# Performance work log

Measured on AMD Instinct MI355X. Metric: run time of the kernel, lower is better.

The kernel has to match this reference:

```python
import jax, jax.numpy as jnp
import numpy as np

HEADS = 4
DIM_HEAD = 128
DIM = 128
INNER = HEADS * DIM_HEAD  # 512
MAX_POS = 100
SCALE = DIM_HEAD ** -0.5


def setup_inputs() -> dict:
    key = jax.random.key(0)
    ks = jax.random.split(key, 8)
    b, h, w = 2, 48, 64
    fmap1 = jax.random.normal(ks[0], (b, DIM, h, w), jnp.float32)
    fmap2 = jax.random.normal(ks[1], (b, DIM, h, w), jnp.float32)
    Wqk = jax.random.normal(ks[2], (2 * INNER, DIM), jnp.float32) * 0.05
    Wv = jax.random.normal(ks[3], (INNER, DIM), jnp.float32) * 0.05
    rel_h = jax.random.normal(ks[4], (2 * MAX_POS - 1, DIM_HEAD), jnp.float32) * 0.05
    rel_w = jax.random.normal(ks[5], (2 * MAX_POS - 1, DIM_HEAD), jnp.float32) * 0.05
    Wp = jax.random.normal(ks[6], (DIM, INNER), jnp.float32) * 0.05
    gamma = jnp.full((1,), 0.1, jnp.float32)  # nonzero so the attn path is active
    return {"fmap1": fmap1, "fmap2": fmap2, "Wqk": Wqk, "Wv": Wv,
            "rel_h": rel_h, "rel_w": rel_w, "Wp": Wp, "gamma": gamma}


def _aggregate(fmap, Wqk, Wv, rel_h, rel_w, Wp, gamma):
    b, c, H, W = fmap.shape
    # 1x1 conv = channel matmul
    qk = jnp.einsum('oc,bchw->bohw', Wqk, fmap)
    q = qk[:, :INNER] * SCALE  # k chunk unused (position-only similarity)
    # b (n d) h w -> b n h w d
    q = q.reshape(b, HEADS, DIM_HEAD, H, W).transpose(0, 1, 3, 4, 2)
    v = jnp.einsum('oc,bchw->bohw', Wv, fmap)
    v = v.reshape(b, HEADS, DIM_HEAD, H, W).transpose(0, 1, 3, 4, 2).reshape(b, HEADS, H * W, DIM_HEAD)
    # relative position similarity (RelPosEmb)
    idx_h = jnp.arange(H)[:, None] - jnp.arange(H)[None, :] + (MAX_POS - 1)  # (H,H)
    idx_w = jnp.arange(W)[:, None] - jnp.arange(W)[None, :] + (MAX_POS - 1)  # (W,W)
    He = rel_h[idx_h]  # (x,u,d)
    We = rel_w[idx_w]  # (y,v,d)
    hs = jnp.einsum('bnxyd,xud->bnxyu', q, He)  # (b,n,x,y,u)
    ws = jnp.einsum('bnxyd,yvd->bnxyv', q, We)  # (b,n,x,y,v)
    sim = hs[..., :, None] + ws[..., None, :]   # (b,n,x,y,u,v)
    sim = sim.reshape(b, HEADS, H * W, H * W)
    attn = jax.nn.softmax(sim, axis=-1)
    out = jnp.einsum('bnij,bnjd->bnid', attn, v)  # (b,n,hw,d)
    out = out.reshape(b, HEADS, H, W, DIM_HEAD).transpose(0, 1, 4, 2, 3).reshape(b, INNER, H, W)
    out = jnp.einsum('oc,bchw->bohw', Wp, out)  # project (dim != inner_dim)
    return fmap + gamma[0] * out


def reference(fmap1, fmap2, Wqk, Wv, rel_h, rel_w, Wp, gamma):
    out1 = _aggregate(fmap1, Wqk, Wv, rel_h, rel_w, Wp, gamma)
    out2 = _aggregate(fmap2, Wqk, Wv, rel_h, rel_w, Wp, gamma)
    return (out1, out2)
```

## Files before the change

kernel.cpp:

```cpp
#include <hip/hip_runtime.h>
#include <cstdint>
#include <cstddef>

typedef short bf16x8 __attribute__((ext_vector_type(8)));
typedef float f32x4 __attribute__((ext_vector_type(4)));

#define HH 48
#define WW 64
#define HWSZ 3072
#define SCALE_Q 0.08838834764831845f

__device__ __forceinline__ float b2f(unsigned short u) {
    union { unsigned int i; float f; } c; c.i = ((unsigned int)u) << 16; return c.f;
}
__device__ __forceinline__ unsigned short f2b(float f) {
    union { float f; unsigned int i; } c; c.f = f;
    unsigned int r = (c.i + 0x7fffu + ((c.i >> 16) & 1u)) >> 16;
    return (unsigned short)r;
}

__device__ __forceinline__ void dma16(const unsigned short* g, unsigned short* l) {
    __builtin_amdgcn_global_load_lds((const __attribute__((address_space(1))) unsigned int*)g,
                                     (__attribute__((address_space(3))) unsigned int*)l,
                                     16, 0, 0);
}

__global__ __launch_bounds__(256) void k_transpose(const float* __restrict__ f0,
                                                   const float* __restrict__ f1,
                                                   unsigned short* __restrict__ Xb) {
    __shared__ float t[32][33];
    int fb = blockIdx.z; int f = fb >> 1, bb = fb & 1;
    const float* src = f ? f1 : f0;
    int pT = blockIdx.x * 32, cT = blockIdx.y * 32;
    int tx = threadIdx.x, ty = threadIdx.y;
#pragma unroll
    for (int i = 0; i < 4; ++i) {
        int c = cT + ty + i * 8, pos = pT + tx;
        t[ty + i * 8][tx] = src[(size_t)(bb * 128 + c) * HWSZ + pos];
    }
    __syncthreads();
#pragma unroll
    for (int i = 0; i < 4; ++i) {
        int pos = pT + ty + i * 8, c = cT + tx;
        Xb[(size_t)(fb * HWSZ + pos) * 128 + c] = f2b(t[tx][ty + i * 8]);
    }
}

__global__ __launch_bounds__(256) void k_weights(const float* __restrict__ Wqk,
                                                 const float* __restrict__ Wv,
                                                 const float* __restrict__ Wp,
                                                 unsigned short* __restrict__ Wcat,
                                                 unsigned short* __restrict__ Wpb) {
    int idx = blockIdx.x * 256 + threadIdx.x;
    if (idx < 131072) {
        int o = idx >> 7, c = idx & 127;
        float v = (o < 512) ? Wqk[o * 128 + c] * SCALE_Q : Wv[(o - 512) * 128 + c];
        Wcat[idx] = f2b(v);
    } else {
        int j = idx - 131072;
        Wpb[j] = f2b(Wp[j]);
    }
}

__global__ __launch_bounds__(256) void k_qv(const unsigned short* __restrict__ Xb,
                                            const unsigned short* __restrict__ Wcat,
                                            unsigned short* __restrict__ Qx,
                                            unsigned short* __restrict__ Vt) {
    __shared__ unsigned short Asub[64 * 136];
    __shared__ unsigned short Bsub[128 * 136];
    int mt = blockIdx.x, nt = blockIdx.y, fb = blockIdx.z;
    int tid = threadIdx.x;
    const unsigned short* asrc = Xb + (size_t)(fb * HWSZ + mt * 64) * 128;
    const unsigned short* bsrc = Wcat + (size_t)nt * 128 * 128;
    for (int ch = tid; ch < 1024; ch += 256) {
        int row = ch >> 4, seg = ch & 15;
        *(bf16x8*)&Asub[row * 136 + seg * 8] = *(const bf16x8*)(asrc + ch * 8);
    }
    for (int ch = tid; ch < 2048; ch += 256) {
        int row = ch >> 4, seg = ch & 15;
        *(bf16x8*)&Bsub[row * 136 + seg * 8] = *(const bf16x8*)(bsrc + ch * 8);
    }
    __syncthreads();
    int l = tid & 63, w = tid >> 6;
    int wm = w >> 1, wn = w & 1;
    int lr = l & 15, lk8 = (l >> 4) * 8;
    f32x4 acc[2][4] = {};
#pragma unroll
    for (int kt = 0; kt < 4; ++kt) {
        bf16x8 a[2], b[4];
#pragma unroll
        for (int m = 0; m < 2; ++m)
            a[m] = *(const bf16x8*)&Asub[(wm * 32 + m * 16 + lr) * 136 + kt * 32 + lk8];
#pragma unroll
        for (int n = 0; n < 4; ++n)
            b[n] = *(const bf16x8*)&Bsub[(wn * 64 + n * 16 + lr) * 136 + kt * 32 + lk8];
#pragma unroll
        for (int m = 0; m < 2; ++m)
#pragma unroll
            for (int n = 0; n < 4; ++n)
                acc[m][n] = __builtin_amdgcn_mfma_f32_16x16x32_bf16(a[m], b[n], acc[m][n], 0, 0, 0);
    }
    int f = fb >> 1, bb = fb & 1;
#pragma unroll
    for (int m = 0; m < 2; ++m)
#pragma unroll
        for (int n = 0; n < 4; ++n) {
            int o = nt * 128 + wn * 64 + n * 16 + lr;
            int pos0 = mt * 64 + wm * 32 + m * 16 + (l >> 4) * 4;
            if (o < 512) {
                int nh = o >> 7, d = o & 127;
#pragma unroll
                for (int r = 0; r < 4; ++r) {
                    int pos = pos0 + r, x = pos >> 6, y = pos & 63;
                    Qx[(size_t)((f * 48 + x) * 512 + (bb * 4 + nh) * 64 + y) * 128 + d] = f2b(acc[m][n][r]);
                }
            } else {
                int oo = o - 512, nh = oo >> 7, d = oo & 127;
                int u = pos0 >> 6, v = pos0 & 63;
                uint2 val;
                val.x = (unsigned int)f2b(acc[m][n][0]) | ((unsigned int)f2b(acc[m][n][1]) << 16);
                val.y = (unsigned int)f2b(acc[m][n][2]) | ((unsigned int)f2b(acc[m][n][3]) << 16);
                *(uint2*)&Vt[(((size_t)(fb * 4 + nh) * 48 + u) * 128 + d) * 64 + v] = val;
            }
        }
}

__global__ __launch_bounds__(256) void k_ph(const unsigned short* __restrict__ Qx,
                                            const float* __restrict__ rel_h,
                                            unsigned short* __restrict__ PH) {
    __shared__ float sm[4][16][52];
    int x = blockIdx.x, f = blockIdx.y, mtz = blockIdx.z;
    int tid = threadIdx.x, l = tid & 63, w = tid >> 6;
    int lr = l & 15, lk8 = (l >> 4) * 8;
    bf16x8 bh[3][4];
#pragma unroll
    for (int ut = 0; ut < 3; ++ut) {
        int u = ut * 16 + lr, rr = x - u + 99;
#pragma unroll
        for (int kt = 0; kt < 4; ++kt) {
            const float* s = rel_h + rr * 128 + kt * 32 + lk8;
            float4 a0 = *(const float4*)s, a1 = *(const float4*)(s + 4);
            bf16x8 pk;
            pk[0] = (short)f2b(a0.x); pk[1] = (short)f2b(a0.y); pk[2] = (short)f2b(a0.z); pk[3] = (short)f2b(a0.w);
            pk[4] = (short)f2b(a1.x); pk[5] = (short)f2b(a1.y); pk[6] = (short)f2b(a1.z); pk[7] = (short)f2b(a1.w);
            bh[ut][kt] = pk;
        }
    }
    const unsigned short* qbase = Qx + (size_t)(f * 48 + x) * 512 * 128;
    unsigned short* phbase = PH + (size_t)(f * 48 + x) * 512 * 48;
    for (int mt = mtz * 2; mt < mtz * 2 + 2; ++mt) {
        int rg = w * 128 + mt * 16 + lr;
        const unsigned short* qrow = qbase + (size_t)rg * 128;
        bf16x8 a[4];
#pragma unroll
        for (int kt = 0; kt < 4; ++kt) a[kt] = *(const bf16x8*)(qrow + kt * 32 + lk8);
        f32x4 acc[3] = {};
#pragma unroll
        for (int kt = 0; kt < 4; ++kt)
#pragma unroll
            for (int ut = 0; ut < 3; ++ut)
                acc[ut] = __builtin_amdgcn_mfma_f32_16x16x32_bf16(a[kt], bh[ut][kt], acc[ut], 0, 0, 0);
        __syncthreads();
#pragma unroll
        for (int ut = 0; ut < 3; ++ut)
#pragma unroll
            for (int r = 0; r < 4; ++r)
                sm[w][(l >> 4) * 4 + r][ut * 16 + lr] = acc[ut][r];
        __syncthreads();
        int part = l >> 4;
        float vb[12];
        float mx = -1e30f;
#pragma unroll
        for (int j = 0; j < 12; ++j) { vb[j] = sm[w][lr][part * 12 + j]; mx = fmaxf(mx, vb[j]); }
        mx = fmaxf(mx, __shfl_xor(mx, 16, 64));
        mx = fmaxf(mx, __shfl_xor(mx, 32, 64));
        float ssum = 0.f;
#pragma unroll
        for (int j = 0; j < 12; ++j) { vb[j] = __expf(vb[j] - mx); ssum += vb[j]; }
        ssum += __shfl_xor(ssum, 16, 64);
        ssum += __shfl_xor(ssum, 32, 64);
        float inv = 1.0f / ssum;
        unsigned short* dst = phbase + (size_t)(w * 128 + mt * 16 + lr) * 48 + part * 12;
#pragma unroll
        for (int j = 0; j < 12; ++j) dst[j] = f2b(vb[j] * inv);
    }
}

__global__ __launch_bounds__(256) void k_pw(const unsigned short* __restrict__ Qx,
                                            const float* __restrict__ rel_w,
                                            unsigned short* __restrict__ PW) {
    __shared__ float sm[4][16][68];
    int y = blockIdx.x, f = blockIdx.y, mtz = blockIdx.z;
    int tid = threadIdx.x, l = tid & 63, w = tid >> 6;
    int lr = l & 15, lk8 = (l >> 4) * 8;
    bf16x8 bw[4][4];
#pragma unroll
    for (int vt = 0; vt < 4; ++vt) {
        int v = vt * 16 + lr, rr = y - v + 99;
#pragma unroll
        for (int kt = 0; kt < 4; ++kt) {
            const float* s = rel_w + rr * 128 + kt * 32 + lk8;
            float4 a0 = *(const float4*)s, a1 = *(const float4*)(s + 4);
            bf16x8 pk;
            pk[0] = (short)f2b(a0.x); pk[1] = (short)f2b(a0.y); pk[2] = (short)f2b(a0.z); pk[3] = (short)f2b(a0.w);
            pk[4] = (short)f2b(a1.x); pk[5] = (short)f2b(a1.y); pk[6] = (short)f2b(a1.z); pk[7] = (short)f2b(a1.w);
            bw[vt][kt] = pk;
        }
    }
    for (int mt = mtz * 2; mt < mtz * 2 + 2; ++mt) {
        int rg = w * 96 + mt * 16 + lr;
        int bn = rg / 48, xx = rg - bn * 48;
        const unsigned short* qrow = Qx + (size_t)((f * 48 + xx) * 512 + bn * 64 + y) * 128;
        bf16x8 a[4];
#pragma unroll
        for (int kt = 0; kt < 4; ++kt) a[kt] = *(const bf16x8*)(qrow + kt * 32 + lk8);
        f32x4 acc[4] = {};
#pragma unroll
        for (int kt = 0; kt < 4; ++kt)
#pragma unroll
            for (int vt = 0; vt < 4; ++vt)
                acc[vt] = __builtin_amdgcn_mfma_f32_16x16x32_bf16(a[kt], bw[vt][kt], acc[vt], 0, 0, 0);
        __syncthreads();
#pragma unroll
        for (int vt = 0; vt < 4; ++vt)
#pragma unroll
            for (int r = 0; r < 4; ++r)
                sm[w][(l >> 4) * 4 + r][vt * 16 + lr] = acc[vt][r];
        __syncthreads();
        int part = l >> 4;
        float vb[16];
        float mx = -1e30f;
#pragma unroll
        for (int j = 0; j < 16; ++j) { vb[j] = sm[w][lr][part * 16 + j]; mx = fmaxf(mx, vb[j]); }
        mx = fmaxf(mx, __shfl_xor(mx, 16, 64));
        mx = fmaxf(mx, __shfl_xor(mx, 32, 64));
        float ssum = 0.f;
#pragma unroll
        for (int j = 0; j < 16; ++j) { vb[j] = __expf(vb[j] - mx); ssum += vb[j]; }
        ssum += __shfl_xor(ssum, 16, 64);
        ssum += __shfl_xor(ssum, 32, 64);
        float inv = 1.0f / ssum;
        unsigned short* dst = PW + (size_t)((f * 64 + y) * 384 + rg) * 64 + part * 16;
#pragma unroll
        for (int j = 0; j < 16; ++j) dst[j] = f2b(vb[j] * inv);
    }
}

__global__ __launch_bounds__(256, 3) void k_attn(const unsigned short* __restrict__ PH,
                                                 const unsigned short* __restrict__ PW,
                                                 const unsigned short* __restrict__ Vt,
                                                 unsigned short* __restrict__ AO) {
    __shared__ unsigned short phl[48 * 128];
    __shared__ unsigned short vbuf[2][4096];
    int bid = blockIdx.x;
    int r16 = bid & 15;
    int rest = bid >> 4;
    int t = rest >> 1, dh = rest & 1;
    int fbn = (r16 & 7) * 2 + (r16 >> 3);
    int f = fbn >> 3, bidx = (fbn >> 2) & 1, nh = fbn & 3;
    int fb = f * 2 + bidx, bn = bidx * 4 + nh;
    int tid = threadIdx.x;
    int l = tid & 63, wd = tid >> 6;
    int lr = l & 15, lg = l >> 4, lk8 = lg * 8;

    const unsigned short* vhalf = Vt + (size_t)(fb * 4 + nh) * 48 * 8192 + dh * 4096;
    int r0 = wd * 16 + (l >> 3), s0 = l & 7;
    int r1 = r0 + 8;
    int g0 = r0 * 64 + ((s0 ^ (r0 & 7)) * 8);
    int g1 = r1 * 64 + ((s0 ^ (r1 & 7)) * 8);

#define DMA_U(BUF, U)                                                           \
    {                                                                           \
        const unsigned short* gt = vhalf + (size_t)(U) * 8192;                  \
        dma16(gt + g0, &vbuf[BUF][wd * 1024]);                                  \
        dma16(gt + g1, &vbuf[BUF][wd * 1024 + 512]);                            \
    }

    DMA_U(0, 0);

    for (int i = tid; i < 3072; i += 256) {
        int up2 = i >> 7, q = i & 127;
        int xy = t * 128 + q, x = xy >> 6, y = xy & 63;
        unsigned int wv = *(const unsigned int*)(PH + ((size_t)(f * 48 + x) * 512 + bn * 64 + y) * 48 + up2 * 2);
        int qoff = (q & 15) * 8 + (q >> 4);
        phl[(up2 * 2) * 128 + qoff]     = (unsigned short)(wv & 0xffffu);
        phl[(up2 * 2 + 1) * 128 + qoff] = (unsigned short)(wv >> 16);
    }
    bf16x8 b[8][2];
#pragma unroll
    for (int n = 0; n < 8; ++n) {
        int xy = t * 128 + n * 16 + lr;
        int x = xy >> 6, y = xy & 63;
        const unsigned short* pwr = PW + ((size_t)(f * 64 + y) * 384 + bn * 48 + x) * 64;
        b[n][0] = *(const bf16x8*)(pwr + lk8);
        b[n][1] = *(const bf16x8*)(pwr + 32 + lk8);
    }
    asm volatile("s_waitcnt vmcnt(0)" ::: "memory");
    __syncthreads();

    int arow = wd * 16 + lr;
    int ao0 = arow * 64 + ((lg ^ (arow & 7)) * 8);
    int ao1 = arow * 64 + (((4 + lg) ^ (arow & 7)) * 8);
    const unsigned short* phrow = &phl[lr * 8];
    f32x4 acc[8] = {};
    const f32x4 zero4 = {0.f, 0.f, 0.f, 0.f};

    int buf = 0;
    for (int u = 0; u < 48; ++u) {
        if (u + 1 < 48) DMA_U(buf ^ 1, u + 1);
        bf16x8 av0 = *(const bf16x8*)&vbuf[buf][ao0];
        bf16x8 av1 = *(const bf16x8*)&vbuf[buf][ao1];
        bf16x8 phv = *(const bf16x8*)(phrow + u * 128);
        __builtin_amdgcn_s_setprio(1);
#pragma unroll
        for (int n = 0; n < 8; ++n) {
            f32x4 Y = __builtin_amdgcn_mfma_f32_16x16x32_bf16(av0, b[n][0], zero4, 0, 0, 0);
            Y = __builtin_amdgcn_mfma_f32_16x16x32_bf16(av1, b[n][1], Y, 0, 0, 0);
            acc[n] += b2f((unsigned short)phv[n]) * Y;
        }
        __builtin_amdgcn_s_setprio(0);
        asm volatile("s_waitcnt vmcnt(0)" ::: "memory");
        __syncthreads();
        buf ^= 1;
    }
#undef DMA_U

    unsigned short* aobase = AO + (size_t)fb * HWSZ * 512 + nh * 128 + dh * 64 + wd * 16 + lg * 4;
#pragma unroll
    for (int n = 0; n < 8; ++n) {
        int q = t * 128 + n * 16 + lr;
        uint2 val;
        val.x = (unsigned int)f2b(acc[n][0]) | ((unsigned int)f2b(acc[n][1]) << 16);
        val.y = (unsigned int)f2b(acc[n][2]) | ((unsigned int)f2b(acc[n][3]) << 16);
        *(uint2*)(aobase + (size_t)q * 512) = val;
    }
}

__global__ __launch_bounds__(256) void k_proj(const unsigned short* __restrict__ AO,
                                              const unsigned short* __restrict__ Wpb,
                                              const float* __restrict__ f0,
                                              const float* __restrict__ f1,
                                              const float* __restrict__ gamma,
                                              float* __restrict__ out) {
    __shared__ unsigned short Asub[32 * 136];
    __shared__ unsigned short Bsub[128 * 136];
    int t = blockIdx.x, fb = blockIdx.y;
    int f = fb >> 1, bb = fb & 1;
    int tid = threadIdx.x;
    int l = tid & 63, w = tid >> 6;
    int wm = w >> 1, wn = w & 1;
    int lr = l & 15, lk8 = (l >> 4) * 8;
    f32x4 acc[4] = {};
    for (int ks = 0; ks < 4; ++ks) {
        if (ks) __syncthreads();
        for (int ch = tid; ch < 512; ch += 256) {
            int row = ch >> 4, seg = ch & 15;
            *(bf16x8*)&Asub[row * 136 + seg * 8] =
                *(const bf16x8*)(AO + (size_t)(fb * HWSZ + t * 32 + row) * 512 + ks * 128 + seg * 8);
        }
        for (int ch = tid; ch < 2048; ch += 256) {
            int row = ch >> 4, seg = ch & 15;
            *(bf16x8*)&Bsub[row * 136 + seg * 8] =
                *(const bf16x8*)(Wpb + (size_t)row * 512 + ks * 128 + seg * 8);
        }
        __syncthreads();
#pragma unroll
        for (int kt = 0; kt < 4; ++kt) {
            bf16x8 a, b[4];
            a = *(const bf16x8*)&Asub[(wm * 16 + lr) * 136 + kt * 32 + lk8];
#pragma unroll
            for (int n = 0; n < 4; ++n)
                b[n] = *(const bf16x8*)&Bsub[(wn * 64 + n * 16 + lr) * 136 + kt * 32 + lk8];
#pragma unroll
            for (int n = 0; n < 4; ++n)
                acc[n] = __builtin_amdgcn_mfma_f32_16x16x32_bf16(a, b[n], acc[n], 0, 0, 0);
        }
    }
    const float* fmapf = f ? f1 : f0;
    float g = gamma[0];
#pragma unroll
    for (int n = 0; n < 4; ++n) {
        int c = wn * 64 + n * 16 + lr;
        int pos0 = t * 32 + wm * 16 + (l >> 4) * 4;
        size_t addr = (size_t)(bb * 128 + c) * HWSZ + pos0;
        float4 fv = *(const float4*)(fmapf + addr);
        float4 ov;
        ov.x = fv.x + g * acc[n][0];
        ov.y = fv.y + g * acc[n][1];
        ov.z = fv.z + g * acc[n][2];
        ov.w = fv.w + g * acc[n][3];
        *(float4*)(out + (size_t)f * 786432 + addr) = ov;
    }
}

extern "C" void kernel_launch(void* const* d_in, const int* in_sizes, int n_in,
                              void* d_out, int out_size, void* d_ws, size_t ws_size,
                              hipStream_t stream) {
    (void)in_sizes; (void)n_in; (void)out_size; (void)ws_size;
    const float* fmap1 = (const float*)d_in[0];
    const float* fmap2 = (const float*)d_in[1];
    const float* Wqk   = (const float*)d_in[2];
    const float* Wv    = (const float*)d_in[3];
    const float* rel_h = (const float*)d_in[4];
    const float* rel_w = (const float*)d_in[5];
    const float* Wp    = (const float*)d_in[6];
    const float* gamma = (const float*)d_in[7];
    float* out = (float*)d_out;
    char* ws = (char*)d_ws;

    unsigned short* Xb   = (unsigned short*)(ws + 0);
    unsigned short* Wcat = (unsigned short*)(ws + 3145728);
    unsigned short* Wpb  = (unsigned short*)(ws + 3407872);
    unsigned short* Qx   = (unsigned short*)(ws + 3538944);
    unsigned short* AO   = Qx;
    unsigned short* Vt   = (unsigned short*)(ws + 16121856);
    unsigned short* PH   = (unsigned short*)(ws + 28704768);
    unsigned short* PW   = (unsigned short*)(ws + 33423360);

    k_transpose<<<dim3(96, 4, 4), dim3(32, 8), 0, stream>>>(fmap1, fmap2, Xb);
    k_weights<<<dim3(768), dim3(256), 0, stream>>>(Wqk, Wv, Wp, Wcat, Wpb);
    k_qv<<<dim3(48, 8, 4), dim3(256), 0, stream>>>(Xb, Wcat, Qx, Vt);
    k_ph<<<dim3(48, 2, 4), dim3(256), 0, stream>>>(Qx, rel_h, PH);
    k_pw<<<dim3(64, 2, 3), dim3(256), 0, stream>>>(Qx, rel_w, PW);
    k_attn<<<dim3(768), dim3(256), 0, stream>>>(PH, PW, Vt, AO);
    k_proj<<<dim3(96, 4), dim3(256), 0, stream>>>(AO, Wpb, fmap1, fmap2, gamma, out);
}
```

Before: 116.7 us.

## Store V in plain channel-major layout and stage via registers instead of LDS DMA

The V projection now writes V as [fb,head,d,HW] instead of a per-row tiled layout. The attention kernel loads each next 64x64 V tile into registers with ordinary global loads and writes it, swizzled, into the alternate LDS buffer after the MFMA work, replacing global_load_lds DMA. The setprio hints are removed. This trades the async DMA path for register staging, which costs extra VGPRs and LDS write instructions and reads strided rows of HWSZ.

```diff
diff --git a/kernel.cpp b/kernel.cpp
--- a/kernel.cpp
+++ b/kernel.cpp
@@ -17,12 +17,6 @@
     union { float f; unsigned int i; } c; c.f = f;
     unsigned int r = (c.i + 0x7fffu + ((c.i >> 16) & 1u)) >> 16;
     return (unsigned short)r;
-}
-
-__device__ __forceinline__ void dma16(const unsigned short* g, unsigned short* l) {
-    __builtin_amdgcn_global_load_lds((const __attribute__((address_space(1))) unsigned int*)g,
-                                     (__attribute__((address_space(3))) unsigned int*)l,
-                                     16, 0, 0);
 }
 
 __global__ __launch_bounds__(256) void k_transpose(const float* __restrict__ f0,
@@ -116,11 +110,10 @@
                 }
             } else {
                 int oo = o - 512, nh = oo >> 7, d = oo & 127;
-                int u = pos0 >> 6, v = pos0 & 63;
                 uint2 val;
                 val.x = (unsigned int)f2b(acc[m][n][0]) | ((unsigned int)f2b(acc[m][n][1]) << 16);
                 val.y = (unsigned int)f2b(acc[m][n][2]) | ((unsigned int)f2b(acc[m][n][3]) << 16);
-                *(uint2*)&Vt[(((size_t)(fb * 4 + nh) * 48 + u) * 128 + d) * 64 + v] = val;
+                *(uint2*)&Vt[(size_t)((fb * 4 + nh) * 128 + d) * HWSZ + pos0] = val;
             }
         }
 }
@@ -251,7 +244,7 @@
                                                  const unsigned short* __restrict__ Vt,
                                                  unsigned short* __restrict__ AO) {
     __shared__ unsigned short phl[48 * 128];
-    __shared__ unsigned short vbuf[2][4096];
+    __shared__ unsigned short vbuf[2][64 * 64];
     int bid = blockIdx.x;
     int r16 = bid & 15;
     int rest = bid >> 4;
@@ -263,20 +256,15 @@
     int l = tid & 63, wd = tid >> 6;
     int lr = l & 15, lg = l >> 4, lk8 = lg * 8;
 
-    const unsigned short* vhalf = Vt + (size_t)(fb * 4 + nh) * 48 * 8192 + dh * 4096;
-    int r0 = wd * 16 + (l >> 3), s0 = l & 7;
-    int r1 = r0 + 8;
-    int g0 = r0 * 64 + ((s0 ^ (r0 & 7)) * 8);
-    int g1 = r1 * 64 + ((s0 ^ (r1 & 7)) * 8);
-
-#define DMA_U(BUF, U)                                                           \
-    {                                                                           \
-        const unsigned short* gt = vhalf + (size_t)(U) * 8192;                  \
-        dma16(gt + g0, &vbuf[BUF][wd * 1024]);                                  \
-        dma16(gt + g1, &vbuf[BUF][wd * 1024 + 512]);                            \
-    }
-
-    DMA_U(0, 0);
+    const unsigned short* vsrc = Vt + (size_t)((fb * 4 + nh) * 128 + dh * 64) * HWSZ;
+    int sd = tid >> 3, sch = tid & 7;
+    const unsigned short* vsrow0 = vsrc + (size_t)sd * HWSZ + sch * 8;
+    const unsigned short* vsrow1 = vsrc + (size_t)(sd + 32) * HWSZ + sch * 8;
+    int wo0 = sd * 64 + ((sch ^ (sd & 7)) * 8);
+    int wo1 = (sd + 32) * 64 + ((sch ^ (sd & 7)) * 8);
+
+    bf16x8 r0a = *(const bf16x8*)(vsrow0);
+    bf16x8 r0b = *(const bf16x8*)(vsrow1);
 
     for (int i = tid; i < 3072; i += 256) {
         int up2 = i >> 7, q = i & 127;
@@ -295,7 +283,8 @@
         b[n][0] = *(const bf16x8*)(pwr + lk8);
         b[n][1] = *(const bf16x8*)(pwr + 32 + lk8);
     }
-    asm volatile("s_waitcnt vmcnt(0)" ::: "memory");
+    *(bf16x8*)&vbuf[0][wo0] = r0a;
+    *(bf16x8*)&vbuf[0][wo1] = r0b;
     __syncthreads();
 
     int arow = wd * 16 + lr;
@@ -304,27 +293,30 @@
     const unsigned short* phrow = &phl[lr * 8];
     f32x4 acc[8] = {};
     const f32x4 zero4 = {0.f, 0.f, 0.f, 0.f};
-
-    int buf = 0;
+    int cur = 0;
     for (int u = 0; u < 48; ++u) {
-        if (u + 1 < 48) DMA_U(buf ^ 1, u + 1);
-        bf16x8 av0 = *(const bf16x8*)&vbuf[buf][ao0];
-        bf16x8 av1 = *(const bf16x8*)&vbuf[buf][ao1];
+        bf16x8 ra, rb;
+        if (u < 47) {
+            ra = *(const bf16x8*)(vsrow0 + (size_t)(u + 1) * 64);
+            rb = *(const bf16x8*)(vsrow1 + (size_t)(u + 1) * 64);
+        }
+        bf16x8 av0 = *(const bf16x8*)&vbuf[cur][ao0];
+        bf16x8 av1 = *(const bf16x8*)&vbuf[cur][ao1];
         bf16x8 phv = *(const bf16x8*)(phrow + u * 128);
-        __builtin_amdgcn_s_setprio(1);
 #pragma unroll
         for (int n = 0; n < 8; ++n) {
             f32x4 Y = __builtin_amdgcn_mfma_f32_16x16x32_bf16(av0, b[n][0], zero4, 0, 0, 0);
             Y = __builtin_amdgcn_mfma_f32_16x16x32_bf16(av1, b[n][1], Y, 0, 0, 0);
-            acc[n] += b2f((unsigned short)phv[n]) * Y;
-        }
-        __builtin_amdgcn_s_setprio(0);
-        asm volatile("s_waitcnt vmcnt(0)" ::: "memory");
-        __syncthreads();
-        buf ^= 1;
-    }
-#undef DMA_U
-
+            float p = b2f((unsigned short)phv[n]);
+            acc[n] += p * Y;
+        }
+        if (u < 47) {
+            *(bf16x8*)&vbuf[cur ^ 1][wo0] = ra;
+            *(bf16x8*)&vbuf[cur ^ 1][wo1] = rb;
+        }
+        __syncthreads();
+        cur ^= 1;
+    }
     unsigned short* aobase = AO + (size_t)fb * HWSZ * 512 + nh * 128 + dh * 64 + wd * 16 + lg * 4;
 #pragma unroll
     for (int n = 0; n < 8; ++n) {
```

New measurement: 111.3 us. -4.6%, faster.
